# Kernel tuning notes

Hardware: AMD Instinct MI355X
Metric: run time of the kernel (lower is better)

## Reference

```python
import jax, jax.numpy as jnp
import numpy as np

START = 1
NUM_CLASSES = 64  # labels drawn from [0, 64)
EPS = 1e-12       # matches F.normalize eps


def _compactness_loss(embeddings, labels):
    # L2-normalize each embedding (F.normalize, dim=-1)
    norms = jnp.maximum(jnp.linalg.norm(embeddings, axis=-1, keepdims=True), EPS)
    emb = embeddings / norms  # [N, D]

    ones = jnp.ones((emb.shape[0],), dtype=emb.dtype)
    counts = jax.ops.segment_sum(ones, labels, num_segments=NUM_CLASSES)      # [C]
    sums = jax.ops.segment_sum(emb, labels, num_segments=NUM_CLASSES)         # [C, D]

    # per-class mean, then L2-normalize the center (F.normalize, dim=1)
    centers = sums / jnp.maximum(counts, 1.0)[:, None]
    c_norms = jnp.maximum(jnp.linalg.norm(centers, axis=-1, keepdims=True), EPS)
    centers = centers / c_norms  # [C, D]

    # cosine similarity of each sample to its own class center
    sim = jnp.sum(emb * centers[labels], axis=-1)  # [N]

    # per-class mean of (1 - sim), only classes with count > 1 contribute
    per_class_sum = jax.ops.segment_sum(1.0 - sim, labels, num_segments=NUM_CLASSES)  # [C]
    valid = counts > 1.0
    class_loss = jnp.where(valid, per_class_sum / jnp.maximum(counts, 1.0), 0.0)
    n_valid = jnp.sum(valid.astype(emb.dtype))
    return jnp.where(n_valid > 0, jnp.sum(class_loss) / jnp.maximum(n_valid, 1.0), 0.0)


def setup_inputs() -> dict:
    key = jax.random.key(0)
    k1, k2 = jax.random.split(key)
    N, D = 262144, 256
    embeddings = jax.random.normal(k1, (N, D), dtype=jnp.float32)
    labels = jax.random.randint(k2, (N,), 0, NUM_CLASSES, dtype=jnp.int64)
    return {"embeddings": embeddings, "labels": labels, "epoch": 5}


def reference(embeddings, labels, epoch):
    if epoch < START:  # epoch is a static python int
        return jnp.asarray(0.0, dtype=embeddings.dtype)
    return _compactness_loss(embeddings, labels)
```

## Files before the change

### kernel.cpp

```cpp
#include <hip/hip_runtime.h>

#define CLS   64
#define DIM   256
#define HB    256
#define HT    256
#define PARTS 8

__device__ __forceinline__ float wave_sum64(float f) {
    int t;
    t = __builtin_amdgcn_update_dpp(0, __float_as_int(f), 0x111, 0xf, 0xf, false); f += __int_as_float(t);
    t = __builtin_amdgcn_update_dpp(0, __float_as_int(f), 0x112, 0xf, 0xf, false); f += __int_as_float(t);
    t = __builtin_amdgcn_update_dpp(0, __float_as_int(f), 0x114, 0xf, 0xe, false); f += __int_as_float(t);
    t = __builtin_amdgcn_update_dpp(0, __float_as_int(f), 0x118, 0xf, 0xc, false); f += __int_as_float(t);
    t = __builtin_amdgcn_update_dpp(0, __float_as_int(f), 0x142, 0xa, 0xf, false); f += __int_as_float(t);
    t = __builtin_amdgcn_update_dpp(0, __float_as_int(f), 0x143, 0xc, 0xf, false); f += __int_as_float(t);
    return __int_as_float(__builtin_amdgcn_readlane(__float_as_int(f), 63));
}

__global__ __launch_bounds__(HT) void k_hist(const int* __restrict__ labels, int N,
                                             int* __restrict__ hist)
{
    __shared__ int h[CLS];
    if (threadIdx.x < CLS) h[threadIdx.x] = 0;
    __syncthreads();
    const int chunk = (N + gridDim.x - 1) / gridDim.x;
    const int s = blockIdx.x * chunk;
    const int e = min(N, s + chunk);
    for (int i = s + threadIdx.x; i < e; i += blockDim.x)
        atomicAdd(&h[labels[i]], 1);
    __syncthreads();
    if (threadIdx.x < CLS) hist[blockIdx.x * CLS + threadIdx.x] = h[threadIdx.x];
}

__global__ __launch_bounds__(HB) void k_scan(int* __restrict__ hist, int* __restrict__ classTot)
{
    __shared__ int a[HB], b[HB];
    const int c = blockIdx.x;
    const int t = threadIdx.x;
    const int v = hist[t * CLS + c];
    a[t] = v;
    __syncthreads();
    int* src = a; int* dst = b;
    for (int off = 1; off < HB; off <<= 1) {
        dst[t] = src[t] + ((t >= off) ? src[t - off] : 0);
        __syncthreads();
        int* tmp = src; src = dst; dst = tmp;
    }
    hist[t * CLS + c] = src[t] - v;
    if (t == HB - 1) classTot[c] = src[t];
}

__global__ __launch_bounds__(HT) void k_scatter(const int* __restrict__ labels, int N,
                                                const int* __restrict__ histEx,
                                                const int* __restrict__ classTot,
                                                int* __restrict__ bucket)
{
    __shared__ int cstart[CLS];
    __shared__ int cur[CLS];
    if (threadIdx.x == 0) {
        int acc = 0;
        for (int j = 0; j < CLS; ++j) { cstart[j] = acc; acc += classTot[j]; }
    }
    __syncthreads();
    if (threadIdx.x < CLS)
        cur[threadIdx.x] = cstart[threadIdx.x] + histEx[blockIdx.x * CLS + threadIdx.x];
    __syncthreads();
    const int chunk = (N + gridDim.x - 1) / gridDim.x;
    const int s = blockIdx.x * chunk;
    const int e = min(N, s + chunk);
    for (int i = s + threadIdx.x; i < e; i += blockDim.x) {
        int c = labels[i];
        int slot = atomicAdd(&cur[c], 1);
        bucket[slot] = i;
    }
}

__global__ __launch_bounds__(1024) void k_classsum(const float* __restrict__ emb,
                                                   const int* __restrict__ bucket,
                                                   const int* __restrict__ classTot,
                                                   float* __restrict__ partials)
{
    __shared__ int cs0, ccnt;
    __shared__ float red[16 * 260];
    const int c    = blockIdx.x / PARTS;
    const int part = blockIdx.x % PARTS;
    if (threadIdx.x == 0) {
        int acc = 0;
        for (int j = 0; j < c; ++j) acc += classTot[j];
        cs0 = acc;
        ccnt = classTot[c];
    }
    __syncthreads();
    const int p0 = cs0 + (int)(((long long)ccnt * part) / PARTS);
    const int p1 = cs0 + (int)(((long long)ccnt * (part + 1)) / PARTS);
    const int wid  = threadIdx.x >> 6;
    const int lane = threadIdx.x & 63;

    float4 acc4 = make_float4(0.f, 0.f, 0.f, 0.f);
    int j = p0 + wid;
    int row = (j < p1) ? bucket[j] : 0;
    while (j < p1) {
        const int jn = j + 16;
        const int rown = (jn < p1) ? bucket[jn] : 0;
        const float4 v = *reinterpret_cast<const float4*>(emb + (size_t)row * DIM + 4 * lane);
        const float ss = wave_sum64(v.x * v.x + v.y * v.y + v.z * v.z + v.w * v.w);
        const float inv = 1.0f / fmaxf(sqrtf(ss), 1e-12f);
        acc4.x += v.x * inv; acc4.y += v.y * inv; acc4.z += v.z * inv; acc4.w += v.w * inv;
        j = jn; row = rown;
    }
    float* my = &red[wid * 260 + 4 * lane];
    my[0] = acc4.x; my[1] = acc4.y; my[2] = acc4.z; my[3] = acc4.w;
    __syncthreads();
    if (threadIdx.x < DIM) {
        float s = 0.f;
        #pragma unroll
        for (int w = 0; w < 16; ++w) s += red[w * 260 + threadIdx.x];
        partials[(size_t)blockIdx.x * DIM + threadIdx.x] = s;
    }
}

__global__ __launch_bounds__(256) void k_classloss(const float* __restrict__ partials,
                                                   const int* __restrict__ classTot,
                                                   float* __restrict__ closs,
                                                   float* __restrict__ cvalid)
{
    const int c = blockIdx.x;
    const int d = threadIdx.x;
    float s = 0.f;
    #pragma unroll
    for (int p = 0; p < PARTS; ++p)
        s += partials[(size_t)(c * PARTS + p) * DIM + d];
    float w = wave_sum64(s * s);
    __shared__ float red[4];
    if ((d & 63) == 0) red[d >> 6] = w;
    __syncthreads();
    if (d == 0) {
        float s2   = red[0] + red[1] + red[2] + red[3];
        float cnt  = (float)classTot[c];
        float invc = 1.0f / fmaxf(cnt, 1.0f);
        float cn   = sqrtf(s2) * invc;
        float dot  = s2 * invc / fmaxf(cn, 1e-12f);
        float pcs  = cnt - dot;
        bool valid = cnt > 1.0f;
        closs[c]  = valid ? pcs * invc : 0.0f;
        cvalid[c] = valid ? 1.0f : 0.0f;
    }
}

__global__ void k_final(const float* __restrict__ closs, const float* __restrict__ cvalid,
                        const int* __restrict__ epoch, float* __restrict__ out)
{
    const int t = threadIdx.x;
    float sl = wave_sum64(closs[t]);
    float nv = wave_sum64(cvalid[t]);
    if (t == 0) {
        float res = (nv > 0.0f) ? (sl / fmaxf(nv, 1.0f)) : 0.0f;
        if (epoch[0] < 1) res = 0.0f;
        out[0] = res;
    }
}

extern "C" void kernel_launch(void* const* d_in, const int* in_sizes, int n_in,
                              void* d_out, int out_size, void* d_ws, size_t ws_size,
                              hipStream_t stream)
{
    const float* emb    = (const float*)d_in[0];
    const int*   labels = (const int*)d_in[1];
    const int*   epoch  = (const int*)d_in[2];
    float*       out    = (float*)d_out;
    const int N = in_sizes[0] / DIM;

    char* ws = (char*)d_ws;
    size_t off = 0;
    auto carve = [&](size_t bytes) { size_t o = off; off = (off + bytes + 255) & ~(size_t)255; return o; };
    int*   hist     = (int*)  (ws + carve((size_t)HB * CLS * sizeof(int)));
    int*   classTot = (int*)  (ws + carve((size_t)CLS * sizeof(int)));
    int*   bucket   = (int*)  (ws + carve((size_t)N * sizeof(int)));
    float* partials = (float*)(ws + carve((size_t)CLS * PARTS * DIM * sizeof(float)));
    float* closs    = (float*)(ws + carve((size_t)CLS * sizeof(float)));
    float* cvalid   = (float*)(ws + carve((size_t)CLS * sizeof(float)));
    (void)ws_size;

    k_hist    <<<HB,          HT,   0, stream>>>(labels, N, hist);
    k_scan    <<<CLS,         HB,   0, stream>>>(hist, classTot);
    k_scatter <<<HB,          HT,   0, stream>>>(labels, N, hist, classTot, bucket);
    k_classsum<<<CLS * PARTS, 1024, 0, stream>>>(emb, bucket, classTot, partials);
    k_classloss<<<CLS,        256,  0, stream>>>(partials, classTot, closs, cvalid);
    k_final   <<<1,           64,   0, stream>>>(closs, cvalid, epoch, out);
}
```

Measured before the change: 62.13 us.

## Fuse histogram and scatter with per-class fixed-capacity buckets, merge loss kernels

Replaces the hist/scan/scatter pipeline with one kernel that reserves per-class offsets through global atomics into a bucket array of capacity N per class, removing the scan kernel and one launch. The class-sum kernel now handles two rows per iteration with nontemporal loads, and the class-loss and final reductions are merged into one single-block kernel. The goal is fewer launches and less serialized small-kernel work. The fat bucket needs CLS*N ints of workspace (64 MB); if the workspace is smaller, the code falls back to the compact path.

```diff
diff --git a/kernel.cpp b/kernel.cpp
--- a/kernel.cpp
+++ b/kernel.cpp
@@ -2,9 +2,12 @@
 
 #define CLS   64
 #define DIM   256
-#define HB    256
-#define HT    256
 #define PARTS 8
+#define HSB   512
+#define HST   256
+#define FB_HB 256
+
+typedef float f32x4 __attribute__((ext_vector_type(4)));
 
 __device__ __forceinline__ float wave_sum64(float f) {
     int t;
@@ -17,8 +20,129 @@
     return __int_as_float(__builtin_amdgcn_readlane(__float_as_int(f), 63));
 }
 
-__global__ __launch_bounds__(HT) void k_hist(const int* __restrict__ labels, int N,
-                                             int* __restrict__ hist)
+template<int CTRL>
+__device__ __forceinline__ float dpp_mov(float x) {
+    return __int_as_float(__builtin_amdgcn_update_dpp(
+        0, __float_as_int(x), CTRL, 0xf, 0xf, true));
+}
+__device__ __forceinline__ float row16_sum(float ss) {
+    ss += dpp_mov<0xB1>(ss);
+    ss += dpp_mov<0x4E>(ss);
+    ss = ss + dpp_mov<0x124>(ss) + dpp_mov<0x128>(ss) + dpp_mov<0x12C>(ss);
+    return ss;
+}
+
+__global__ void k_zero(int* __restrict__ p) { p[threadIdx.x] = 0; }
+
+__global__ __launch_bounds__(HST) void k_histscatter(
+    const int* __restrict__ labels, int N, int cap,
+    int* __restrict__ classCnt, int* __restrict__ bucket)
+{
+    __shared__ int h[CLS];
+    __shared__ int cur[CLS];
+    const int tid = threadIdx.x;
+    if (tid < CLS) h[tid] = 0;
+    __syncthreads();
+    const int chunk = (N + gridDim.x - 1) / gridDim.x;
+    const int s = blockIdx.x * chunk;
+    const int e = min(N, s + chunk);
+    for (int i = s + tid; i < e; i += HST)
+        atomicAdd(&h[labels[i]], 1);
+    __syncthreads();
+    if (tid < CLS) cur[tid] = atomicAdd(&classCnt[tid], h[tid]);
+    __syncthreads();
+    for (int i = s + tid; i < e; i += HST) {
+        int c = labels[i];
+        int pos = atomicAdd(&cur[c], 1);
+        bucket[(size_t)c * cap + pos] = i;
+    }
+}
+
+__global__ __launch_bounds__(1024) void k_classsum(
+    const float* __restrict__ emb, const int* __restrict__ bucket,
+    const int* __restrict__ classCnt, int cap, float* __restrict__ partials)
+{
+    __shared__ float red[16 * 260];
+    const int c    = blockIdx.x >> 3;
+    const int part = blockIdx.x & (PARTS - 1);
+    const int ccnt = classCnt[c];
+    const int p0 = (int)(((long long)ccnt * part) / PARTS);
+    const int p1 = (int)(((long long)ccnt * (part + 1)) / PARTS);
+    const int* bkt = bucket + (size_t)c * cap;
+    const int wid  = threadIdx.x >> 6;
+    const int lane = threadIdx.x & 63;
+
+    f32x4 acc = {0.f, 0.f, 0.f, 0.f};
+    for (int j = p0 + 2 * wid; j < p1; j += 32) {
+        const int rA = bkt[j];
+        const bool hasB = (j + 1 < p1);
+        const int rB = hasB ? bkt[j + 1] : rA;
+        const f32x4 a = __builtin_nontemporal_load(
+            reinterpret_cast<const f32x4*>(emb + (size_t)rA * DIM) + lane);
+        const f32x4 b = __builtin_nontemporal_load(
+            reinterpret_cast<const f32x4*>(emb + (size_t)rB * DIM) + lane);
+        const float sA = wave_sum64(a.x*a.x + a.y*a.y + a.z*a.z + a.w*a.w);
+        const float iA = 1.0f / fmaxf(sqrtf(sA), 1e-12f);
+        acc.x += a.x * iA; acc.y += a.y * iA; acc.z += a.z * iA; acc.w += a.w * iA;
+        const float sB = wave_sum64(b.x*b.x + b.y*b.y + b.z*b.z + b.w*b.w);
+        if (hasB) {
+            const float iB = 1.0f / fmaxf(sqrtf(sB), 1e-12f);
+            acc.x += b.x * iB; acc.y += b.y * iB; acc.z += b.z * iB; acc.w += b.w * iB;
+        }
+    }
+    float* my = &red[wid * 260 + 4 * lane];
+    my[0] = acc.x; my[1] = acc.y; my[2] = acc.z; my[3] = acc.w;
+    __syncthreads();
+    if (threadIdx.x < DIM) {
+        float s = 0.f;
+        #pragma unroll
+        for (int w = 0; w < 16; ++w) s += red[w * 260 + threadIdx.x];
+        partials[(size_t)blockIdx.x * DIM + threadIdx.x] = s;
+    }
+}
+
+__global__ __launch_bounds__(1024) void k_lossfinal(
+    const float* __restrict__ partials, const int* __restrict__ classCnt,
+    const int* __restrict__ epoch, float* __restrict__ out)
+{
+    __shared__ float closs[CLS], cvalid[CLS];
+    const int tid = threadIdx.x;
+    const int c = tid >> 4;
+    const int k = tid & 15;
+    float s2loc = 0.f;
+    for (int dd = 0; dd < 16; ++dd) {
+        const int d = k * 16 + dd;
+        float v = 0.f;
+        #pragma unroll
+        for (int p = 0; p < PARTS; ++p)
+            v += partials[(size_t)(c * PARTS + p) * DIM + d];
+        s2loc += v * v;
+    }
+    const float s2 = row16_sum(s2loc);
+    if (k == 0) {
+        float cnt  = (float)classCnt[c];
+        float invc = 1.0f / fmaxf(cnt, 1.0f);
+        float cn   = sqrtf(s2) * invc;
+        float dot  = s2 * invc / fmaxf(cn, 1e-12f);
+        float pcs  = cnt - dot;
+        bool valid = cnt > 1.0f;
+        closs[c]  = valid ? pcs * invc : 0.0f;
+        cvalid[c] = valid ? 1.0f : 0.0f;
+    }
+    __syncthreads();
+    if (tid < 64) {
+        float sl = wave_sum64(closs[tid]);
+        float nv = wave_sum64(cvalid[tid]);
+        if (tid == 0) {
+            float res = (nv > 0.0f) ? (sl / fmaxf(nv, 1.0f)) : 0.0f;
+            if (epoch[0] < 1) res = 0.0f;
+            out[0] = res;
+        }
+    }
+}
+
+__global__ __launch_bounds__(HST) void k_hist(const int* __restrict__ labels, int N,
+                                              int* __restrict__ hist)
 {
     __shared__ int h[CLS];
     if (threadIdx.x < CLS) h[threadIdx.x] = 0;
@@ -32,38 +156,36 @@
     if (threadIdx.x < CLS) hist[blockIdx.x * CLS + threadIdx.x] = h[threadIdx.x];
 }
 
-__global__ __launch_bounds__(HB) void k_scan(int* __restrict__ hist, int* __restrict__ classTot)
-{
-    __shared__ int a[HB], b[HB];
-    const int c = blockIdx.x;
-    const int t = threadIdx.x;
+__global__ __launch_bounds__(FB_HB) void k_scan(int* __restrict__ hist, int* __restrict__ classTot)
+{
+    __shared__ int a[FB_HB], b[FB_HB];
+    const int c = blockIdx.x, t = threadIdx.x;
     const int v = hist[t * CLS + c];
     a[t] = v;
     __syncthreads();
     int* src = a; int* dst = b;
-    for (int off = 1; off < HB; off <<= 1) {
+    for (int off = 1; off < FB_HB; off <<= 1) {
         dst[t] = src[t] + ((t >= off) ? src[t - off] : 0);
         __syncthreads();
         int* tmp = src; src = dst; dst = tmp;
     }
     hist[t * CLS + c] = src[t] - v;
-    if (t == HB - 1) classTot[c] = src[t];
-}
-
-__global__ __launch_bounds__(HT) void k_scatter(const int* __restrict__ labels, int N,
-                                                const int* __restrict__ histEx,
-                                                const int* __restrict__ classTot,
-                                                int* __restrict__ bucket)
-{
-    __shared__ int cstart[CLS];
+    if (t == FB_HB - 1) classTot[c] = src[t];
+}
+
+__global__ __launch_bounds__(HST) void k_scatter(const int* __restrict__ labels, int N,
+                                                 const int* __restrict__ histEx,
+                                                 const int* __restrict__ classTot,
+                                                 int* __restrict__ bucket)
+{
     __shared__ int cur[CLS];
     if (threadIdx.x == 0) {
         int acc = 0;
-        for (int j = 0; j < CLS; ++j) { cstart[j] = acc; acc += classTot[j]; }
+        for (int j = 0; j < CLS; ++j) { cur[j] = acc; acc += classTot[j]; }
     }
     __syncthreads();
     if (threadIdx.x < CLS)
-        cur[threadIdx.x] = cstart[threadIdx.x] + histEx[blockIdx.x * CLS + threadIdx.x];
+        cur[threadIdx.x] += histEx[blockIdx.x * CLS + threadIdx.x];
     __syncthreads();
     const int chunk = (N + gridDim.x - 1) / gridDim.x;
     const int s = blockIdx.x * chunk;
@@ -75,41 +197,33 @@
     }
 }
 
-__global__ __launch_bounds__(1024) void k_classsum(const float* __restrict__ emb,
-                                                   const int* __restrict__ bucket,
-                                                   const int* __restrict__ classTot,
-                                                   float* __restrict__ partials)
+__global__ __launch_bounds__(1024) void k_classsum_compact(
+    const float* __restrict__ emb, const int* __restrict__ bucket,
+    const int* __restrict__ classTot, float* __restrict__ partials)
 {
     __shared__ int cs0, ccnt;
     __shared__ float red[16 * 260];
-    const int c    = blockIdx.x / PARTS;
-    const int part = blockIdx.x % PARTS;
+    const int c    = blockIdx.x >> 3;
+    const int part = blockIdx.x & (PARTS - 1);
     if (threadIdx.x == 0) {
         int acc = 0;
         for (int j = 0; j < c; ++j) acc += classTot[j];
-        cs0 = acc;
-        ccnt = classTot[c];
+        cs0 = acc; ccnt = classTot[c];
     }
     __syncthreads();
     const int p0 = cs0 + (int)(((long long)ccnt * part) / PARTS);
     const int p1 = cs0 + (int)(((long long)ccnt * (part + 1)) / PARTS);
-    const int wid  = threadIdx.x >> 6;
-    const int lane = threadIdx.x & 63;
-
-    float4 acc4 = make_float4(0.f, 0.f, 0.f, 0.f);
-    int j = p0 + wid;
-    int row = (j < p1) ? bucket[j] : 0;
-    while (j < p1) {
-        const int jn = j + 16;
-        const int rown = (jn < p1) ? bucket[jn] : 0;
-        const float4 v = *reinterpret_cast<const float4*>(emb + (size_t)row * DIM + 4 * lane);
-        const float ss = wave_sum64(v.x * v.x + v.y * v.y + v.z * v.z + v.w * v.w);
+    const int wid = threadIdx.x >> 6, lane = threadIdx.x & 63;
+    f32x4 acc = {0.f, 0.f, 0.f, 0.f};
+    for (int j = p0 + wid; j < p1; j += 16) {
+        const int row = bucket[j];
+        const f32x4 v = *(reinterpret_cast<const f32x4*>(emb + (size_t)row * DIM) + lane);
+        const float ss = wave_sum64(v.x*v.x + v.y*v.y + v.z*v.z + v.w*v.w);
         const float inv = 1.0f / fmaxf(sqrtf(ss), 1e-12f);
-        acc4.x += v.x * inv; acc4.y += v.y * inv; acc4.z += v.z * inv; acc4.w += v.w * inv;
-        j = jn; row = rown;
+        acc.x += v.x * inv; acc.y += v.y * inv; acc.z += v.z * inv; acc.w += v.w * inv;
     }
     float* my = &red[wid * 260 + 4 * lane];
-    my[0] = acc4.x; my[1] = acc4.y; my[2] = acc4.z; my[3] = acc4.w;
+    my[0] = acc.x; my[1] = acc.y; my[2] = acc.z; my[3] = acc.w;
     __syncthreads();
     if (threadIdx.x < DIM) {
         float s = 0.f;
@@ -119,46 +233,6 @@
     }
 }
 
-__global__ __launch_bounds__(256) void k_classloss(const float* __restrict__ partials,
-                                                   const int* __restrict__ classTot,
-                                                   float* __restrict__ closs,
-                                                   float* __restrict__ cvalid)
-{
-    const int c = blockIdx.x;
-    const int d = threadIdx.x;
-    float s = 0.f;
-    #pragma unroll
-    for (int p = 0; p < PARTS; ++p)
-        s += partials[(size_t)(c * PARTS + p) * DIM + d];
-    float w = wave_sum64(s * s);
-    __shared__ float red[4];
-    if ((d & 63) == 0) red[d >> 6] = w;
-    __syncthreads();
-    if (d == 0) {
-        float s2   = red[0] + red[1] + red[2] + red[3];
-        float cnt  = (float)classTot[c];
-        float invc = 1.0f / fmaxf(cnt, 1.0f);
-        float cn   = sqrtf(s2) * invc;
-        float dot  = s2 * invc / fmaxf(cn, 1e-12f);
-        float pcs  = cnt - dot;
-        bool valid = cnt > 1.0f;
-        closs[c]  = valid ? pcs * invc : 0.0f;
-        cvalid[c] = valid ? 1.0f : 0.0f;
-    }
-}
-
-__global__ void k_final(const float* __restrict__ closs, const float* __restrict__ cvalid,
-                        const int* __restrict__ epoch, float* __restrict__ out)
-{
-    const int t = threadIdx.x;
-    float sl = wave_sum64(closs[t]);
-    float nv = wave_sum64(cvalid[t]);
-    if (t == 0) {
-        float res = (nv > 0.0f) ? (sl / fmaxf(nv, 1.0f)) : 0.0f;
-        if (epoch[0] < 1) res = 0.0f;
-        out[0] = res;
-    }
-}
 
 extern "C" void kernel_launch(void* const* d_in, const int* in_sizes, int n_in,
                               void* d_out, int out_size, void* d_ws, size_t ws_size,
@@ -173,18 +247,23 @@
     char* ws = (char*)d_ws;
     size_t off = 0;
     auto carve = [&](size_t bytes) { size_t o = off; off = (off + bytes + 255) & ~(size_t)255; return o; };
-    int*   hist     = (int*)  (ws + carve((size_t)HB * CLS * sizeof(int)));
-    int*   classTot = (int*)  (ws + carve((size_t)CLS * sizeof(int)));
+    int*   classCnt = (int*)  (ws + carve((size_t)CLS * sizeof(int)));
+    float* partials = (float*)(ws + carve((size_t)CLS * PARTS * DIM * sizeof(float)));
+    int*   hist     = (int*)  (ws + carve((size_t)FB_HB * CLS * sizeof(int)));
     int*   bucket   = (int*)  (ws + carve((size_t)N * sizeof(int)));
-    float* partials = (float*)(ws + carve((size_t)CLS * PARTS * DIM * sizeof(float)));
-    float* closs    = (float*)(ws + carve((size_t)CLS * sizeof(float)));
-    float* cvalid   = (float*)(ws + carve((size_t)CLS * sizeof(float)));
-    (void)ws_size;
-
-    k_hist    <<<HB,          HT,   0, stream>>>(labels, N, hist);
-    k_scan    <<<CLS,         HB,   0, stream>>>(hist, classTot);
-    k_scatter <<<HB,          HT,   0, stream>>>(labels, N, hist, classTot, bucket);
-    k_classsum<<<CLS * PARTS, 1024, 0, stream>>>(emb, bucket, classTot, partials);
-    k_classloss<<<CLS,        256,  0, stream>>>(partials, classTot, closs, cvalid);
-    k_final   <<<1,           64,   0, stream>>>(closs, cvalid, epoch, out);
-}
+    size_t fbEnd = off;
+    int*   bucketFat = (int*) (ws + carve((size_t)CLS * N * sizeof(int)));
+
+    if (ws_size >= off) {
+        k_zero       <<<1,           CLS,  0, stream>>>(classCnt);
+        k_histscatter<<<HSB,         HST,  0, stream>>>(labels, N, N, classCnt, bucketFat);
+        k_classsum   <<<CLS * PARTS, 1024, 0, stream>>>(emb, bucketFat, classCnt, N, partials);
+        k_lossfinal  <<<1,           1024, 0, stream>>>(partials, classCnt, epoch, out);
+    } else if (ws_size >= fbEnd) {
+        k_hist      <<<FB_HB,       HST,   0, stream>>>(labels, N, hist);
+        k_scan      <<<CLS,         FB_HB, 0, stream>>>(hist, classCnt);
+        k_scatter   <<<FB_HB,       HST,   0, stream>>>(labels, N, hist, classCnt, bucket);
+        k_classsum_compact<<<CLS * PARTS, 1024, 0, stream>>>(emb, bucket, classCnt, partials);
+        k_lossfinal <<<1,           1024,  0, stream>>>(partials, classCnt, epoch, out);
+    }
+}
```

New measurement: 77.72 us. +25.1%, slower.

## Fuse class histogram scan into scatter kernel and precompute class start offsets

Applied to the files above, without the earlier changes.

Removes the separate scan kernel. Each scatter block now recomputes its per-class prefix and the class totals directly from the histogram, and block 0 writes a class-start array. The class-sum kernel reads start offsets from that array instead of serially summing class totals in one thread. The bucket-index prefetch in the class-sum loop is also dropped. This saves one kernel launch and a serial loop, but every scatter block redundantly reads the full histogram.

```diff
diff --git a/kernel.cpp b/kernel.cpp
--- a/kernel.cpp
+++ b/kernel.cpp
@@ -2,9 +2,11 @@
 
 #define CLS   64
 #define DIM   256
+#define PARTS 8
 #define HB    256
 #define HT    256
-#define PARTS 8
+
+typedef float f32x4 __attribute__((ext_vector_type(4)));
 
 __device__ __forceinline__ float wave_sum64(float f) {
     int t;
@@ -32,84 +34,73 @@
     if (threadIdx.x < CLS) hist[blockIdx.x * CLS + threadIdx.x] = h[threadIdx.x];
 }
 
-__global__ __launch_bounds__(HB) void k_scan(int* __restrict__ hist, int* __restrict__ classTot)
+__global__ __launch_bounds__(HT) void k_scatter2(
+    const int* __restrict__ labels, int N,
+    const int* __restrict__ hist,
+    int* __restrict__ cstart,
+    int* __restrict__ bucket)
 {
-    __shared__ int a[HB], b[HB];
-    const int c = blockIdx.x;
-    const int t = threadIdx.x;
-    const int v = hist[t * CLS + c];
-    a[t] = v;
+    __shared__ int t4[4][CLS], p4[4][CLS];
+    __shared__ int tot[CLS], pre[CLS], cur[CLS];
+    const int tid = threadIdx.x;
+    const int c = tid & 63, q = tid >> 6;
+    int t = 0, p = 0;
+    const int myb = blockIdx.x;
+    #pragma unroll 4
+    for (int b = q * (HB / 4); b < (q + 1) * (HB / 4); ++b) {
+        const int v = hist[b * CLS + c];
+        t += v;
+        if (b < myb) p += v;
+    }
+    t4[q][c] = t; p4[q][c] = p;
     __syncthreads();
-    int* src = a; int* dst = b;
-    for (int off = 1; off < HB; off <<= 1) {
-        dst[t] = src[t] + ((t >= off) ? src[t - off] : 0);
-        __syncthreads();
-        int* tmp = src; src = dst; dst = tmp;
-    }
-    hist[t * CLS + c] = src[t] - v;
-    if (t == HB - 1) classTot[c] = src[t];
-}
-
-__global__ __launch_bounds__(HT) void k_scatter(const int* __restrict__ labels, int N,
-                                                const int* __restrict__ histEx,
-                                                const int* __restrict__ classTot,
-                                                int* __restrict__ bucket)
-{
-    __shared__ int cstart[CLS];
-    __shared__ int cur[CLS];
-    if (threadIdx.x == 0) {
-        int acc = 0;
-        for (int j = 0; j < CLS; ++j) { cstart[j] = acc; acc += classTot[j]; }
+    if (tid < CLS) {
+        tot[tid] = t4[0][tid] + t4[1][tid] + t4[2][tid] + t4[3][tid];
+        pre[tid] = p4[0][tid] + p4[1][tid] + p4[2][tid] + p4[3][tid];
     }
     __syncthreads();
-    if (threadIdx.x < CLS)
-        cur[threadIdx.x] = cstart[threadIdx.x] + histEx[blockIdx.x * CLS + threadIdx.x];
+    if (tid == 0) {
+        int acc = 0;
+        for (int j = 0; j < CLS; ++j) { cur[j] = acc + pre[j]; acc += tot[j]; }
+    }
     __syncthreads();
+    if (myb == 0) {
+        if (tid < CLS) cstart[tid] = cur[tid] - pre[tid];
+        if (tid == CLS) cstart[CLS] = N;
+    }
     const int chunk = (N + gridDim.x - 1) / gridDim.x;
-    const int s = blockIdx.x * chunk;
+    const int s = myb * chunk;
     const int e = min(N, s + chunk);
-    for (int i = s + threadIdx.x; i < e; i += blockDim.x) {
-        int c = labels[i];
-        int slot = atomicAdd(&cur[c], 1);
+    for (int i = s + tid; i < e; i += HT) {
+        const int cc = labels[i];
+        const int slot = atomicAdd(&cur[cc], 1);
         bucket[slot] = i;
     }
 }
 
-__global__ __launch_bounds__(1024) void k_classsum(const float* __restrict__ emb,
-                                                   const int* __restrict__ bucket,
-                                                   const int* __restrict__ classTot,
-                                                   float* __restrict__ partials)
+__global__ __launch_bounds__(1024) void k_classsum(
+    const float* __restrict__ emb, const int* __restrict__ bucket,
+    const int* __restrict__ cstart, float* __restrict__ partials)
 {
-    __shared__ int cs0, ccnt;
     __shared__ float red[16 * 260];
-    const int c    = blockIdx.x / PARTS;
-    const int part = blockIdx.x % PARTS;
-    if (threadIdx.x == 0) {
-        int acc = 0;
-        for (int j = 0; j < c; ++j) acc += classTot[j];
-        cs0 = acc;
-        ccnt = classTot[c];
-    }
-    __syncthreads();
-    const int p0 = cs0 + (int)(((long long)ccnt * part) / PARTS);
-    const int p1 = cs0 + (int)(((long long)ccnt * (part + 1)) / PARTS);
-    const int wid  = threadIdx.x >> 6;
-    const int lane = threadIdx.x & 63;
+    const int c    = blockIdx.x >> 3;
+    const int part = blockIdx.x & (PARTS - 1);
+    const int s0 = cstart[c], s1 = cstart[c + 1];
+    const int ccnt = s1 - s0;
+    const int p0 = s0 + (int)(((long long)ccnt * part) >> 3);
+    const int p1 = s0 + (int)(((long long)ccnt * (part + 1)) >> 3);
+    const int wid = threadIdx.x >> 6, lane = threadIdx.x & 63;
 
-    float4 acc4 = make_float4(0.f, 0.f, 0.f, 0.f);
-    int j = p0 + wid;
-    int row = (j < p1) ? bucket[j] : 0;
-    while (j < p1) {
-        const int jn = j + 16;
-        const int rown = (jn < p1) ? bucket[jn] : 0;
-        const float4 v = *reinterpret_cast<const float4*>(emb + (size_t)row * DIM + 4 * lane);
+    f32x4 acc = {0.f, 0.f, 0.f, 0.f};
+    for (int j = p0 + wid; j < p1; j += 16) {
+        const int row = bucket[j];
+        const f32x4 v = *(reinterpret_cast<const f32x4*>(emb + (size_t)row * DIM) + lane);
         const float ss = wave_sum64(v.x * v.x + v.y * v.y + v.z * v.z + v.w * v.w);
         const float inv = 1.0f / fmaxf(sqrtf(ss), 1e-12f);
-        acc4.x += v.x * inv; acc4.y += v.y * inv; acc4.z += v.z * inv; acc4.w += v.w * inv;
-        j = jn; row = rown;
+        acc.x += v.x * inv; acc.y += v.y * inv; acc.z += v.z * inv; acc.w += v.w * inv;
     }
     float* my = &red[wid * 260 + 4 * lane];
-    my[0] = acc4.x; my[1] = acc4.y; my[2] = acc4.z; my[3] = acc4.w;
+    my[0] = acc.x; my[1] = acc.y; my[2] = acc.z; my[3] = acc.w;
     __syncthreads();
     if (threadIdx.x < DIM) {
         float s = 0.f;
@@ -119,10 +110,9 @@
     }
 }
 
-__global__ __launch_bounds__(256) void k_classloss(const float* __restrict__ partials,
-                                                   const int* __restrict__ classTot,
-                                                   float* __restrict__ closs,
-                                                   float* __restrict__ cvalid)
+__global__ __launch_bounds__(256) void k_classloss(
+    const float* __restrict__ partials, const int* __restrict__ cstart,
+    float* __restrict__ closs, float* __restrict__ cvalid)
 {
     const int c = blockIdx.x;
     const int d = threadIdx.x;
@@ -130,13 +120,13 @@
     #pragma unroll
     for (int p = 0; p < PARTS; ++p)
         s += partials[(size_t)(c * PARTS + p) * DIM + d];
-    float w = wave_sum64(s * s);
+    const float w = wave_sum64(s * s);
     __shared__ float red[4];
     if ((d & 63) == 0) red[d >> 6] = w;
     __syncthreads();
     if (d == 0) {
         float s2   = red[0] + red[1] + red[2] + red[3];
-        float cnt  = (float)classTot[c];
+        float cnt  = (float)(cstart[c + 1] - cstart[c]);
         float invc = 1.0f / fmaxf(cnt, 1.0f);
         float cn   = sqrtf(s2) * invc;
         float dot  = s2 * invc / fmaxf(cn, 1e-12f);
@@ -151,8 +141,8 @@
                         const int* __restrict__ epoch, float* __restrict__ out)
 {
     const int t = threadIdx.x;
-    float sl = wave_sum64(closs[t]);
-    float nv = wave_sum64(cvalid[t]);
+    const float sl = wave_sum64(closs[t]);
+    const float nv = wave_sum64(cvalid[t]);
     if (t == 0) {
         float res = (nv > 0.0f) ? (sl / fmaxf(nv, 1.0f)) : 0.0f;
         if (epoch[0] < 1) res = 0.0f;
@@ -174,17 +164,16 @@
     size_t off = 0;
     auto carve = [&](size_t bytes) { size_t o = off; off = (off + bytes + 255) & ~(size_t)255; return o; };
     int*   hist     = (int*)  (ws + carve((size_t)HB * CLS * sizeof(int)));
-    int*   classTot = (int*)  (ws + carve((size_t)CLS * sizeof(int)));
+    int*   cstart   = (int*)  (ws + carve((size_t)(CLS + 1) * sizeof(int)));
     int*   bucket   = (int*)  (ws + carve((size_t)N * sizeof(int)));
     float* partials = (float*)(ws + carve((size_t)CLS * PARTS * DIM * sizeof(float)));
     float* closs    = (float*)(ws + carve((size_t)CLS * sizeof(float)));
     float* cvalid   = (float*)(ws + carve((size_t)CLS * sizeof(float)));
     (void)ws_size;
 
-    k_hist    <<<HB,          HT,   0, stream>>>(labels, N, hist);
-    k_scan    <<<CLS,         HB,   0, stream>>>(hist, classTot);
-    k_scatter <<<HB,          HT,   0, stream>>>(labels, N, hist, classTot, bucket);
-    k_classsum<<<CLS * PARTS, 1024, 0, stream>>>(emb, bucket, classTot, partials);
-    k_classloss<<<CLS,        256,  0, stream>>>(partials, classTot, closs, cvalid);
-    k_final   <<<1,           64,   0, stream>>>(closs, cvalid, epoch, out);
+    k_hist     <<<HB,          HT,   0, stream>>>(labels, N, hist);
+    k_scatter2 <<<HB,          HT,   0, stream>>>(labels, N, hist, cstart, bucket);
+    k_classsum <<<CLS * PARTS, 1024, 0, stream>>>(emb, bucket, cstart, partials);
+    k_classloss<<<CLS,         256,  0, stream>>>(partials, cstart, closs, cvalid);
+    k_final    <<<1,           64,   0, stream>>>(closs, cvalid, epoch, out);
 }
```

Measured after the change: 61.78 us. No clear change (-0.6%).
